# Kernel tuning notes

Measured on AMD Instinct MI355X. Metric: run time of the kernel, lower is better.

## Reference

```python
import jax, jax.numpy as jnp
import numpy as np

B, S, D, HD = 32, 1024, 768, 64  # batch, seq, d_model, head_dim (= d_model // num_heads)


def setup_inputs() -> dict:
    key = jax.random.key(0)
    ks = jax.random.split(key, 4)
    x = jax.random.normal(ks[0], (B, S, D), dtype=jnp.float32)
    # Linear weights stored as [in, out]; init scaled like torch default (~1/sqrt(in))
    scale = 1.0 / np.sqrt(D)
    Wq = jax.random.normal(ks[1], (D, HD), dtype=jnp.float32) * scale
    Wk = jax.random.normal(ks[2], (D, HD), dtype=jnp.float32) * scale
    Wv = jax.random.normal(ks[3], (D, HD), dtype=jnp.float32) * scale
    bq = jnp.zeros((HD,), dtype=jnp.float32)
    bk = jnp.zeros((HD,), dtype=jnp.float32)
    bv = jnp.zeros((HD,), dtype=jnp.float32)
    return {"x": x, "Wq": Wq, "bq": bq, "Wk": Wk, "bk": bk, "Wv": Wv, "bv": bv}


def reference(x, Wq, bq, Wk, bk, Wv, bv):
    # q, k, v: [B, S, HD]
    q = jnp.einsum("bsd,dh->bsh", x, Wq) + bq
    k = jnp.einsum("bsd,dh->bsh", x, Wk) + bk
    v = jnp.einsum("bsd,dh->bsh", x, Wv) + bv
    # NOTE: module scales by 1/d_model (not 1/sqrt(head_dim)) — kept faithful.
    scores = jnp.einsum("bqh,bkh->bqk", q, k) / jnp.asarray(D, q.dtype)
    attn = jax.nn.softmax(scores, axis=-1)  # [B, S, S]
    # dropout is identity at inference (attn_drop treated as eval mode)
    return jnp.einsum("bqk,bkh->bqh", attn, v)
```

## Files before the change

kernel.cpp:

```cpp
#include <hip/hip_runtime.h>
#include <hip/hip_bf16.h>


constexpr int NB = 32;
constexpr int NS = 1024;
constexpr int ND = 768;
constexpr int NH = 64;
constexpr float SC2 = (1.0f / 768.0f) * 1.4426950408889634f;

typedef __attribute__((ext_vector_type(8))) short bf16x8;
typedef __attribute__((ext_vector_type(4))) float f32x4;
typedef __attribute__((ext_vector_type(16))) float f32x16;
typedef __attribute__((ext_vector_type(4))) unsigned int u32x4;

__device__ __forceinline__ unsigned short f2bf(float f) {
    unsigned int u = __float_as_uint(f);
    u += 0x7FFFu + ((u >> 16) & 1u);
    return (unsigned short)(u >> 16);
}

__device__ __forceinline__ unsigned int pkbf(float lo, float hi) {
    __hip_bfloat162 h = __float22bfloat162_rn(float2{lo, hi});
    return *reinterpret_cast<unsigned int*>(&h);
}

__device__ __forceinline__ void pl32swap(unsigned int a, unsigned int b,
                                         unsigned int& x, unsigned int& y) {
    auto r = __builtin_amdgcn_permlane32_swap((int)a, (int)b, false, false);
    x = (unsigned int)r[0];
    y = (unsigned int)r[1];
}

__device__ __forceinline__ float xswap_add(float v) {
    unsigned int a, b;
    pl32swap(__float_as_uint(v), __float_as_uint(v), a, b);
    return __uint_as_float(a) + __uint_as_float(b);
}

__global__ void wtrans_kernel(const float* __restrict__ Wq, const float* __restrict__ Wk,
                              const float* __restrict__ Wv, short* __restrict__ Wtf) {
    int idx = blockIdx.x * 256 + threadIdx.x;
    int f = idx >> 9, q = idx & 511;
    int lane = q >> 3, e = q & 7;
    int ln = lane & 15, g = lane >> 4;
    int nt = f / 24, ks = f - nt * 24;
    int n = nt * 16 + ln;
    int k = ks * 32 + g * 8 + e;
    const float* W = (n < 64) ? Wq : ((n < 128) ? Wk : Wv);
    Wtf[idx] = (short)f2bf(W[(size_t)k * NH + (n & 63)]);
}

__global__ __launch_bounds__(256, 3) void qkv_kernel(
    const float* __restrict__ x, const short* __restrict__ Wtf,
    const float* __restrict__ bq, const float* __restrict__ bk, const float* __restrict__ bv,
    short* __restrict__ Qw, short* __restrict__ Kw, short* __restrict__ Vwt)
{
    __shared__ __align__(16) short As[32 * 776];

    const int t = threadIdx.x;
    const int wi = t >> 6, lane = t & 63, ln = lane & 15, g = lane >> 4;
    const int m0 = blockIdx.x * 32;
    const float* xblk = x + (size_t)m0 * ND;

    float4 ld[24];
    #pragma unroll
    for (int j = 0; j < 24; j++)
        ld[j] = *(const float4*)(xblk + (j * 256 + t) * 4);
    #pragma unroll
    for (int j = 0; j < 24; j++) {
        int p = (j * 256 + t) * 4;
        int row = p / ND, col = p - row * ND;
        unsigned int u0 = pkbf(ld[j].x, ld[j].y);
        unsigned int u1 = pkbf(ld[j].z, ld[j].w);
        *(uint2*)&As[row * 776 + col] = uint2{u0, u1};
    }
    __syncthreads();

    f32x4 acc[2][3];
    #pragma unroll
    for (int i = 0; i < 2; i++)
        #pragma unroll
        for (int j = 0; j < 3; j++) acc[i][j] = f32x4{0.f, 0.f, 0.f, 0.f};

    const short* bbase = Wtf + (size_t)(wi * 3) * 24 * 512 + lane * 8;

    #pragma unroll 4
    for (int ks = 0; ks < 24; ks++) {
        bf16x8 bfr[3];
        #pragma unroll
        for (int nf = 0; nf < 3; nf++)
            bfr[nf] = *(const bf16x8*)(bbase + (nf * 24 + ks) * 512);
        bf16x8 af[2];
        #pragma unroll
        for (int mf = 0; mf < 2; mf++)
            af[mf] = *(const bf16x8*)&As[(mf * 16 + ln) * 776 + ks * 32 + g * 8];
        #pragma unroll
        for (int mf = 0; mf < 2; mf++)
            #pragma unroll
            for (int nf = 0; nf < 3; nf++)
                acc[mf][nf] = __builtin_amdgcn_mfma_f32_16x16x32_bf16(
                    af[mf], bfr[nf], acc[mf][nf], 0, 0, 0);
    }

    #pragma unroll
    for (int nf = 0; nf < 3; nf++) {
        int n = wi * 48 + nf * 16 + ln;
        int mat = n >> 6, col = n & 63;
        const float* bp = (mat == 0) ? bq : ((mat == 1) ? bk : bv);
        float bias = bp[col];
        #pragma unroll
        for (int mf = 0; mf < 2; mf++) {
            int rbase = m0 + mf * 16 + g * 4;
            #pragma unroll
            for (int r = 0; r < 4; r++) {
                float v = acc[mf][nf][r] + bias;
                int row = rbase + r;
                if (mat == 0) {
                    Qw[(size_t)row * NH + col] = (short)f2bf(v * SC2);
                } else if (mat == 1) {
                    Kw[(size_t)row * NH + col] = (short)f2bf(v);
                } else {
                    int bb = row >> 10, ss = row & 1023;
                    Vwt[((size_t)bb * NH + col) * NS + ss] = (short)f2bf(v);
                }
            }
        }
    }
}

__global__ __launch_bounds__(512, 4) void attn_kernel(
    const short* __restrict__ Qw, const short* __restrict__ Kw,
    const short* __restrict__ Vwt, float* __restrict__ out)
{
    __shared__ __align__(16) short sm[4][2][64][72];

    const int t = threadIdx.x;
    const int w = t >> 6;
    const int lane = t & 63, l31 = lane & 31, h32 = lane >> 5;
    const int gk = w >> 1, wq = w & 1;
    const int b = blockIdx.y, qt = blockIdx.x;

    short (*Ks)[72] = sm[gk][0];
    short (*Vs)[72] = sm[gk][1];

    const short* qbase = Qw + ((size_t)(b * NS + qt * 64 + wq * 32 + l31)) * NH + h32 * 8;
    bf16x8 qf[4];
    #pragma unroll
    for (int ks = 0; ks < 4; ks++) qf[ks] = *(const bf16x8*)(qbase + ks * 16);

    f32x16 oacc[2];
    #pragma unroll
    for (int i = 0; i < 16; i++) { oacc[0][i] = 0.f; oacc[1][i] = 0.f; }
    float l_part = 0.f;

    const int tg = t & 127;
    const int srow = tg >> 1, scb = (tg & 1) * 32;
    const int key00 = gk * 256;
    const short* ksrc = Kw + ((size_t)(b * NS + key00 + srow)) * NH + scb;
    const short* vsrc = Vwt + ((size_t)(b * NH + srow)) * NS + key00 + scb;

    bf16x8 kpre[4], vpre[4];
    #pragma unroll
    for (int i = 0; i < 4; i++) {
        kpre[i] = *(const bf16x8*)(ksrc + i * 8);
        vpre[i] = *(const bf16x8*)(vsrc + i * 8);
    }
    #pragma unroll
    for (int i = 0; i < 4; i++) {
        *(bf16x8*)&Ks[srow][scb + i * 8] = kpre[i];
        *(bf16x8*)&Vs[srow][scb + i * 8] = vpre[i];
    }
    __syncthreads();

    constexpr int NT = 4;
    for (int kt = 0; kt < NT; kt++) {
        if (kt < NT - 1) {
            const short* kp = ksrc + (size_t)(kt + 1) * 64 * NH;
            const short* vp = vsrc + (kt + 1) * 64;
            #pragma unroll
            for (int i = 0; i < 4; i++) {
                kpre[i] = *(const bf16x8*)(kp + i * 8);
                vpre[i] = *(const bf16x8*)(vp + i * 8);
            }
        }

        float sl = 0.f;
        u32x4 pw[4];

        {
            f32x16 st;
            #pragma unroll
            for (int i = 0; i < 16; i++) st[i] = 0.f;
            __builtin_amdgcn_s_setprio(1);
            #pragma unroll
            for (int ks = 0; ks < 4; ks++) {
                bf16x8 a0 = *(const bf16x8*)&Ks[l31][ks * 16 + h32 * 8];
                st = __builtin_amdgcn_mfma_f32_32x32x16_bf16(a0, qf[ks], st, 0, 0, 0);
            }
            __builtin_amdgcn_s_setprio(0);
            #pragma unroll
            for (int i = 0; i < 16; i++) { st[i] = exp2f(st[i]); sl += st[i]; }
            unsigned int c[8];
            #pragma unroll
            for (int i = 0; i < 8; i++) c[i] = pkbf(st[2 * i], st[2 * i + 1]);
            unsigned int w0, w1, w2, w3;
            pl32swap(c[0], c[2], w0, w2); pl32swap(c[1], c[3], w1, w3);
            pw[0] = u32x4{w0, w1, w2, w3};
            pl32swap(c[4], c[6], w0, w2); pl32swap(c[5], c[7], w1, w3);
            pw[1] = u32x4{w0, w1, w2, w3};
        }
        {
            f32x16 st;
            #pragma unroll
            for (int i = 0; i < 16; i++) st[i] = 0.f;
            __builtin_amdgcn_s_setprio(1);
            #pragma unroll
            for (int ks = 0; ks < 4; ks++) {
                bf16x8 a1 = *(const bf16x8*)&Ks[32 + l31][ks * 16 + h32 * 8];
                st = __builtin_amdgcn_mfma_f32_32x32x16_bf16(a1, qf[ks], st, 0, 0, 0);
            }
            __builtin_amdgcn_s_setprio(0);
            #pragma unroll
            for (int i = 0; i < 16; i++) { st[i] = exp2f(st[i]); sl += st[i]; }
            unsigned int c[8];
            #pragma unroll
            for (int i = 0; i < 8; i++) c[i] = pkbf(st[2 * i], st[2 * i + 1]);
            unsigned int w0, w1, w2, w3;
            pl32swap(c[0], c[2], w0, w2); pl32swap(c[1], c[3], w1, w3);
            pw[2] = u32x4{w0, w1, w2, w3};
            pl32swap(c[4], c[6], w0, w2); pl32swap(c[5], c[7], w1, w3);
            pw[3] = u32x4{w0, w1, w2, w3};
        }
        l_part += sl;

        __builtin_amdgcn_s_setprio(1);
        #pragma unroll
        for (int ks = 0; ks < 4; ks++) {
            bf16x8 pb = *(bf16x8*)&pw[ks];
            #pragma unroll
            for (int ht = 0; ht < 2; ht++) {
                bf16x8 va = *(const bf16x8*)&Vs[ht * 32 + l31][ks * 16 + h32 * 8];
                oacc[ht] = __builtin_amdgcn_mfma_f32_32x32x16_bf16(va, pb, oacc[ht], 0, 0, 0);
            }
        }
        __builtin_amdgcn_s_setprio(0);

        if (kt < NT - 1) {
            __syncthreads();
            #pragma unroll
            for (int i = 0; i < 4; i++) {
                *(bf16x8*)&Ks[srow][scb + i * 8] = kpre[i];
                *(bf16x8*)&Vs[srow][scb + i * 8] = vpre[i];
            }
            __syncthreads();
        }
    }

    float l_run = xswap_add(l_part);
    __syncthreads();
    float* mg = (float*)&sm[0][0][0][0];
    constexpr int SLOT = 64 * 69;
    constexpr int LBASE = 3 * SLOT;
    const int qloc = wq * 32 + l31;
    if (gk > 0) {
        float* ob = mg + (gk - 1) * SLOT + qloc * 69;
        #pragma unroll
        for (int ht = 0; ht < 2; ht++)
            #pragma unroll
            for (int r = 0; r < 16; r++)
                ob[ht * 32 + (r & 3) + 8 * (r >> 2) + 4 * h32] = oacc[ht][r];
        if (h32 == 0) mg[LBASE + (gk - 1) * 64 + qloc] = l_run;
    }
    __syncthreads();
    if (gk == 0) {
        float l_tot = l_run + mg[LBASE + qloc] + mg[LBASE + 64 + qloc] + mg[LBASE + 128 + qloc];
        float linv = 1.0f / l_tot;
        float* op = out + ((size_t)(b * NS + qt * 64 + qloc)) * NH;
        const float* o1 = mg + qloc * 69;
        #pragma unroll
        for (int ht = 0; ht < 2; ht++)
            #pragma unroll
            for (int r = 0; r < 16; r++) {
                int hv = ht * 32 + (r & 3) + 8 * (r >> 2) + 4 * h32;
                float s = oacc[ht][r] + o1[hv] + o1[SLOT + hv] + o1[2 * SLOT + hv];
                op[hv] = s * linv;
            }
    }
}

extern "C" void kernel_launch(void* const* d_in, const int* in_sizes, int n_in,
                              void* d_out, int out_size, void* d_ws, size_t ws_size,
                              hipStream_t stream)
{
    const float* x  = (const float*)d_in[0];
    const float* Wq = (const float*)d_in[1];
    const float* bq = (const float*)d_in[2];
    const float* Wk = (const float*)d_in[3];
    const float* bk = (const float*)d_in[4];
    const float* Wv = (const float*)d_in[5];
    const float* bv = (const float*)d_in[6];
    float* out = (float*)d_out;

    const size_t qkv_elems = (size_t)NB * NS * NH;
    short* Qw  = (short*)d_ws;
    short* Kw  = Qw + qkv_elems;
    short* Vwt = Kw + qkv_elems;
    short* Wtf = Vwt + qkv_elems;

    wtrans_kernel<<<576, 256, 0, stream>>>(Wq, Wk, Wv, Wtf);
    qkv_kernel<<<(NB * NS) / 32, 256, 0, stream>>>(x, Wtf, bq, bk, bv, Qw, Kw, Vwt);
    attn_kernel<<<dim3(NS / 64, NB), 512, 0, stream>>>(Qw, Kw, Vwt, out);
}
```

Baseline: 66.55 us.

## Load x fragments directly from global in QKV projection, drop LDS staging

```diff
diff --git a/kernel.cpp b/kernel.cpp
--- a/kernel.cpp
+++ b/kernel.cpp
@@ -50,31 +50,18 @@
     Wtf[idx] = (short)f2bf(W[(size_t)k * NH + (n & 63)]);
 }
 
-__global__ __launch_bounds__(256, 3) void qkv_kernel(
+__global__ __launch_bounds__(256, 4) void qkv_kernel(
     const float* __restrict__ x, const short* __restrict__ Wtf,
     const float* __restrict__ bq, const float* __restrict__ bk, const float* __restrict__ bv,
     short* __restrict__ Qw, short* __restrict__ Kw, short* __restrict__ Vwt)
 {
-    __shared__ __align__(16) short As[32 * 776];
-
     const int t = threadIdx.x;
     const int wi = t >> 6, lane = t & 63, ln = lane & 15, g = lane >> 4;
     const int m0 = blockIdx.x * 32;
-    const float* xblk = x + (size_t)m0 * ND;
-
-    float4 ld[24];
-    #pragma unroll
-    for (int j = 0; j < 24; j++)
-        ld[j] = *(const float4*)(xblk + (j * 256 + t) * 4);
-    #pragma unroll
-    for (int j = 0; j < 24; j++) {
-        int p = (j * 256 + t) * 4;
-        int row = p / ND, col = p - row * ND;
-        unsigned int u0 = pkbf(ld[j].x, ld[j].y);
-        unsigned int u1 = pkbf(ld[j].z, ld[j].w);
-        *(uint2*)&As[row * 776 + col] = uint2{u0, u1};
-    }
-    __syncthreads();
+
+    const float* ar0 = x + (size_t)(m0 + ln) * ND + g * 8;
+    const float* ar1 = ar0 + (size_t)16 * ND;
+    const short* bbase = Wtf + (size_t)(wi * 3) * 24 * 512 + lane * 8;
 
     f32x4 acc[2][3];
     #pragma unroll
@@ -82,24 +69,29 @@
         #pragma unroll
         for (int j = 0; j < 3; j++) acc[i][j] = f32x4{0.f, 0.f, 0.f, 0.f};
 
-    const short* bbase = Wtf + (size_t)(wi * 3) * 24 * 512 + lane * 8;
-
-    #pragma unroll 4
+    #pragma unroll 2
     for (int ks = 0; ks < 24; ks++) {
-        bf16x8 bfr[3];
-        #pragma unroll
-        for (int nf = 0; nf < 3; nf++)
-            bfr[nf] = *(const bf16x8*)(bbase + (nf * 24 + ks) * 512);
-        bf16x8 af[2];
-        #pragma unroll
-        for (int mf = 0; mf < 2; mf++)
-            af[mf] = *(const bf16x8*)&As[(mf * 16 + ln) * 776 + ks * 32 + g * 8];
-        #pragma unroll
-        for (int mf = 0; mf < 2; mf++)
-            #pragma unroll
-            for (int nf = 0; nf < 3; nf++)
-                acc[mf][nf] = __builtin_amdgcn_mfma_f32_16x16x32_bf16(
-                    af[mf], bfr[nf], acc[mf][nf], 0, 0, 0);
+        float4 a00 = *(const float4*)(ar0 + ks * 32);
+        float4 a01 = *(const float4*)(ar0 + ks * 32 + 4);
+        float4 a10 = *(const float4*)(ar1 + ks * 32);
+        float4 a11 = *(const float4*)(ar1 + ks * 32 + 4);
+        bf16x8 b0 = *(const bf16x8*)(bbase + (0 * 24 + ks) * 512);
+        bf16x8 b1 = *(const bf16x8*)(bbase + (1 * 24 + ks) * 512);
+        bf16x8 b2 = *(const bf16x8*)(bbase + (2 * 24 + ks) * 512);
+
+        u32x4 v0{pkbf(a00.x, a00.y), pkbf(a00.z, a00.w),
+                 pkbf(a01.x, a01.y), pkbf(a01.z, a01.w)};
+        u32x4 v1{pkbf(a10.x, a10.y), pkbf(a10.z, a10.w),
+                 pkbf(a11.x, a11.y), pkbf(a11.z, a11.w)};
+        bf16x8 af0 = *reinterpret_cast<bf16x8*>(&v0);
+        bf16x8 af1 = *reinterpret_cast<bf16x8*>(&v1);
+
+        acc[0][0] = __builtin_amdgcn_mfma_f32_16x16x32_bf16(af0, b0, acc[0][0], 0, 0, 0);
+        acc[0][1] = __builtin_amdgcn_mfma_f32_16x16x32_bf16(af0, b1, acc[0][1], 0, 0, 0);
+        acc[0][2] = __builtin_amdgcn_mfma_f32_16x16x32_bf16(af0, b2, acc[0][2], 0, 0, 0);
+        acc[1][0] = __builtin_amdgcn_mfma_f32_16x16x32_bf16(af1, b0, acc[1][0], 0, 0, 0);
+        acc[1][1] = __builtin_amdgcn_mfma_f32_16x16x32_bf16(af1, b1, acc[1][1], 0, 0, 0);
+        acc[1][2] = __builtin_amdgcn_mfma_f32_16x16x32_bf16(af1, b2, acc[1][2], 0, 0, 0);
     }
 
     #pragma unroll
```

Measured after the change: 90.24 us. +35.6%, slower.

## Stream x through K-tiled LDS with register prefetch in QKV projection

Applied to the files above, without the earlier changes.

```diff
diff --git a/kernel.cpp b/kernel.cpp
--- a/kernel.cpp
+++ b/kernel.cpp
@@ -50,31 +50,22 @@
     Wtf[idx] = (short)f2bf(W[(size_t)k * NH + (n & 63)]);
 }
 
-__global__ __launch_bounds__(256, 3) void qkv_kernel(
+__global__ __launch_bounds__(512, 4) void qkv_kernel(
     const float* __restrict__ x, const short* __restrict__ Wtf,
     const float* __restrict__ bq, const float* __restrict__ bk, const float* __restrict__ bv,
     short* __restrict__ Qw, short* __restrict__ Kw, short* __restrict__ Vwt)
 {
-    __shared__ __align__(16) short As[32 * 776];
+    __shared__ __align__(16) short As[64][72];
 
     const int t = threadIdx.x;
-    const int wi = t >> 6, lane = t & 63, ln = lane & 15, g = lane >> 4;
-    const int m0 = blockIdx.x * 32;
-    const float* xblk = x + (size_t)m0 * ND;
-
-    float4 ld[24];
-    #pragma unroll
-    for (int j = 0; j < 24; j++)
-        ld[j] = *(const float4*)(xblk + (j * 256 + t) * 4);
-    #pragma unroll
-    for (int j = 0; j < 24; j++) {
-        int p = (j * 256 + t) * 4;
-        int row = p / ND, col = p - row * ND;
-        unsigned int u0 = pkbf(ld[j].x, ld[j].y);
-        unsigned int u1 = pkbf(ld[j].z, ld[j].w);
-        *(uint2*)&As[row * 776 + col] = uint2{u0, u1};
-    }
-    __syncthreads();
+    const int w = t >> 6, lane = t & 63, ln = lane & 15, g = lane >> 4;
+    const int wm = w >> 2, wn = w & 3;
+    const int m0 = blockIdx.x * 64;
+
+    const int srow = t >> 3, scol = (t & 7) * 8;
+    const float* xr = x + (size_t)(m0 + srow) * ND + scol;
+
+    const short* bbase = Wtf + (size_t)(wn * 3) * 24 * 512 + lane * 8;
 
     f32x4 acc[2][3];
     #pragma unroll
@@ -82,35 +73,58 @@
         #pragma unroll
         for (int j = 0; j < 3; j++) acc[i][j] = f32x4{0.f, 0.f, 0.f, 0.f};
 
-    const short* bbase = Wtf + (size_t)(wi * 3) * 24 * 512 + lane * 8;
-
-    #pragma unroll 4
-    for (int ks = 0; ks < 24; ks++) {
-        bf16x8 bfr[3];
-        #pragma unroll
-        for (int nf = 0; nf < 3; nf++)
-            bfr[nf] = *(const bf16x8*)(bbase + (nf * 24 + ks) * 512);
-        bf16x8 af[2];
+    float4 xp0 = *(const float4*)(xr);
+    float4 xp1 = *(const float4*)(xr + 4);
+
+    #pragma unroll 1
+    for (int kt = 0; kt < 12; kt++) {
+        __syncthreads();
+        {
+            u32x4 v{pkbf(xp0.x, xp0.y), pkbf(xp0.z, xp0.w),
+                    pkbf(xp1.x, xp1.y), pkbf(xp1.z, xp1.w)};
+            *(u32x4*)&As[srow][scol] = v;
+        }
+        __syncthreads();
+
+        if (kt < 11) {
+            xp0 = *(const float4*)(xr + (kt + 1) * 64);
+            xp1 = *(const float4*)(xr + (kt + 1) * 64 + 4);
+        }
+
+        bf16x8 b0[3], b1[3];
+        #pragma unroll
+        for (int nf = 0; nf < 3; nf++) {
+            b0[nf] = *(const bf16x8*)(bbase + (nf * 24 + kt * 2) * 512);
+            b1[nf] = *(const bf16x8*)(bbase + (nf * 24 + kt * 2 + 1) * 512);
+        }
+        bf16x8 af0[2], af1[2];
+        #pragma unroll
+        for (int mf = 0; mf < 2; mf++) {
+            af0[mf] = *(const bf16x8*)&As[wm * 32 + mf * 16 + ln][g * 8];
+            af1[mf] = *(const bf16x8*)&As[wm * 32 + mf * 16 + ln][32 + g * 8];
+        }
+        __builtin_amdgcn_s_setprio(1);
         #pragma unroll
         for (int mf = 0; mf < 2; mf++)
-            af[mf] = *(const bf16x8*)&As[(mf * 16 + ln) * 776 + ks * 32 + g * 8];
-        #pragma unroll
-        for (int mf = 0; mf < 2; mf++)
-            #pragma unroll
-            for (int nf = 0; nf < 3; nf++)
+            #pragma unroll
+            for (int nf = 0; nf < 3; nf++) {
                 acc[mf][nf] = __builtin_amdgcn_mfma_f32_16x16x32_bf16(
-                    af[mf], bfr[nf], acc[mf][nf], 0, 0, 0);
+                    af0[mf], b0[nf], acc[mf][nf], 0, 0, 0);
+                acc[mf][nf] = __builtin_amdgcn_mfma_f32_16x16x32_bf16(
+                    af1[mf], b1[nf], acc[mf][nf], 0, 0, 0);
+            }
+        __builtin_amdgcn_s_setprio(0);
     }
 
     #pragma unroll
     for (int nf = 0; nf < 3; nf++) {
-        int n = wi * 48 + nf * 16 + ln;
+        int n = wn * 48 + nf * 16 + ln;
         int mat = n >> 6, col = n & 63;
         const float* bp = (mat == 0) ? bq : ((mat == 1) ? bk : bv);
         float bias = bp[col];
         #pragma unroll
         for (int mf = 0; mf < 2; mf++) {
-            int rbase = m0 + mf * 16 + g * 4;
+            int rbase = m0 + wm * 32 + mf * 16 + g * 4;
             #pragma unroll
             for (int r = 0; r < 4; r++) {
                 float v = acc[mf][nf][r] + bias;
@@ -308,6 +322,6 @@
     short* Wtf = Vwt + qkv_elems;
 
     wtrans_kernel<<<576, 256, 0, stream>>>(Wq, Wk, Wv, Wtf);
-    qkv_kernel<<<(NB * NS) / 32, 256, 0, stream>>>(x, Wtf, bq, bk, bv, Qw, Kw, Vwt);
+    qkv_kernel<<<(NB * NS) / 64, 512, 0, stream>>>(x, Wtf, bq, bk, bv, Qw, Kw, Vwt);
     attn_kernel<<<dim3(NS / 64, NB), 512, 0, stream>>>(Qw, Kw, Vwt, out);
 }
```

Result: faster. 62.53 us (-6.0%).
